# Performance work log

Measured on AMD Instinct MI355X. Metric: run time of the kernel, lower is better.

The kernel has to match this reference:

```python
import jax, jax.numpy as jnp
import numpy as np

B, EIN, GIN, LAT, E = 32768, 128, 64, 16, 8
H1, H2, H3 = 512, 256, 128          # CpExpertNet hidden_sizes
BB, GH = 128, 128                   # gate backbone_dim, gating_hidden_dim
EPS = 1e-5

def _ln(x, g, b):
    # LayerNorm over last dim (eps=1e-5, affine)
    mu = jnp.mean(x, axis=-1, keepdims=True)
    var = jnp.mean(jnp.square(x - mu), axis=-1, keepdims=True)
    return (x - mu) * jax.lax.rsqrt(var + EPS) * g + b

def setup_inputs() -> dict:
    key = jax.random.key(0)
    ks = iter(jax.random.split(key, 64))
    def p(shape, s=0.05):
        return jax.random.normal(next(ks), shape, jnp.float32) * s
    inp = dict(
        expert_features=jax.random.normal(next(ks), (B, EIN), jnp.float32),
        gate_features=jax.random.normal(next(ks), (B, GIN), jnp.float32),
        # stacked expert params (E parallel MLPs: in->512->256->128->1, LN after each hidden Linear)
        eW1=p((E, EIN, H1)), eb1=p((E, H1)), eg1=jnp.ones((E, H1), jnp.float32), ebt1=jnp.zeros((E, H1), jnp.float32),
        eW2=p((E, H1, H2)), eb2=p((E, H2)), eg2=jnp.ones((E, H2), jnp.float32), ebt2=jnp.zeros((E, H2), jnp.float32),
        eW3=p((E, H2, H3)), eb3=p((E, H3)), eg3=jnp.ones((E, H3), jnp.float32), ebt3=jnp.zeros((E, H3), jnp.float32),
        eW4=p((E, H3, 1)), eb4=p((E, 1)),
        # gate backbone: Linear(GIN,BB)+LN+SiLU, Linear(BB,BB)+LN+SiLU
        bW1=p((GIN, BB)), bb1=p((BB,)), bg1=jnp.ones((BB,), jnp.float32), bbt1=jnp.zeros((BB,), jnp.float32),
        bW2=p((BB, BB)), bb2=p((BB,)), bg2=jnp.ones((BB,), jnp.float32), bbt2=jnp.zeros((BB,), jnp.float32),
        # encoder: Linear(BB,BB//2)+SiLU, Linear(BB//2,LAT)
        encW1=p((BB, BB // 2)), encb1=p((BB // 2,)), encW2=p((BB // 2, LAT)), encb2=p((LAT,)),
        # gating: Linear(BB+LAT,GH)+LN+SiLU+(Dropout eval), Linear(GH,GH//2)+SiLU, Linear(GH//2,E)
        gW1=p((BB + LAT, GH)), gb1=p((GH,)), gg1=jnp.ones((GH,), jnp.float32), gbt1=jnp.zeros((GH,), jnp.float32),
        gW2=p((GH, GH // 2)), gb2=p((GH // 2,)),
        gW3=p((GH // 2, E)), gb3=p((E,)),
    )
    return inp

def reference(expert_features, gate_features,
              eW1, eb1, eg1, ebt1, eW2, eb2, eg2, ebt2, eW3, eb3, eg3, ebt3, eW4, eb4,
              bW1, bb1, bg1, bbt1, bW2, bb2, bg2, bbt2,
              encW1, encb1, encW2, encb2,
              gW1, gb1, gg1, gbt1, gW2, gb2, gW3, gb3):
    silu = jax.nn.silu
    # --- LatentGateNet ---
    h = silu(_ln(gate_features @ bW1 + bb1, bg1, bbt1))
    h = silu(_ln(h @ bW2 + bb2, bg2, bbt2))            # [B, BB]
    z = silu(h @ encW1 + encb1) @ encW2 + encb2        # [B, LAT]
    g = silu(_ln(jnp.concatenate([h, z], axis=1) @ gW1 + gb1, gg1, gbt1))
    g = silu(g @ gW2 + gb2)
    logits = g @ gW3 + gb3                             # [B, E]
    gates = jax.nn.softmax(logits, axis=1)
    # --- experts, batched over E via einsum (dropout is identity in eval) ---
    x = silu(_ln(jnp.einsum('bi,eih->beh', expert_features, eW1) + eb1, eg1, ebt1))  # [B,E,512]
    x = silu(_ln(jnp.einsum('beh,ehk->bek', x, eW2) + eb2, eg2, ebt2))               # [B,E,256]
    x = silu(_ln(jnp.einsum('bek,ekm->bem', x, eW3) + eb3, eg3, ebt3))               # [B,E,128]
    out = jnp.einsum('bem,emo->beo', x, eW4) + eb4                                   # [B,E,1]
    stacked = jnp.transpose(out, (0, 2, 1))                                          # [B,1,E]
    mixed = jnp.sum(stacked * gates[:, None, :], axis=2)                             # [B,1]
    return (mixed, z, logits, gates)
```

## Files before the change

kernel.cpp:

```cpp
#include <hip/hip_runtime.h>
#include <hip/hip_bf16.h>


typedef __attribute__((ext_vector_type(8))) short bf16x8;
typedef __attribute__((ext_vector_type(4))) short bf16x4;
typedef __attribute__((ext_vector_type(4))) float f32x4;

#define DEV static __device__ __forceinline__

DEV float b2f(unsigned short u){ union { unsigned int i; float f; } x; x.i = ((unsigned int)u) << 16; return x.f; }
DEV unsigned short f2b(float f){
  union { float f; unsigned int i; } x; x.f = f;
  return (unsigned short)((x.i + 0x7fffu + ((x.i >> 16) & 1u)) >> 16);
}
DEV unsigned int pk2(float a, float b){
  __hip_bfloat162 h = __float22bfloat162_rn(make_float2(a, b));
  union { __hip_bfloat162 h; unsigned int u; } u; u.h = h; return u.u;
}
DEV float silu_f(float v){ return v / (1.0f + __expf(-v)); }


__global__ __launch_bounds__(256) void pack_x_kernel(const float* __restrict__ X, unsigned short* __restrict__ Xp){
  int t = blockIdx.x * 256 + threadIdx.x;
  int l = t & 63, kb = (t >> 6) & 3, mtg = t >> 8;
  int row = mtg * 16 + (l & 15);
  int k0  = kb * 32 + (l >> 4) * 8;
  const float* src = X + (size_t)row * 128 + k0;
  bf16x8 o;
  #pragma unroll
  for (int j = 0; j < 8; j++) o[j] = (short)f2b(src[j]);
  *(bf16x8*)(Xp + (size_t)t * 8) = o;
}

__global__ __launch_bounds__(256) void pack_w_kernel(const float* __restrict__ eW1, const float* __restrict__ eW2,
                                                     const float* __restrict__ eW3, const float* __restrict__ eW4,
                                                     unsigned short* __restrict__ W1p, unsigned short* __restrict__ W2p,
                                                     unsigned short* __restrict__ W3p, float* __restrict__ w4p){
  int b = blockIdx.x;
  if (b < 256){
    int t = b * 256 + threadIdx.x;
    int l = t & 63, kb = (t >> 6) & 3, ntg = (t >> 8) & 31, e = t >> 13;
    int q = l >> 4, c0 = l & 15, n = ntg * 16 + c0;
    bf16x8 o;
    #pragma unroll
    for (int j = 0; j < 8; j++){ int k = kb*32 + q*8 + j; o[j] = (short)f2b(eW1[((size_t)e*128 + k)*512 + n]); }
    *(bf16x8*)(W1p + (size_t)t * 8) = o;
  } else if (b < 768){
    int t = (b - 256) * 256 + threadIdx.x;
    int l = t & 63, kb = (t >> 6) & 15, ntg = (t >> 10) & 15, e = t >> 14;
    int q = l >> 4, c0 = l & 15, n = ntg * 16 + c0;
    bf16x8 o;
    #pragma unroll
    for (int j = 0; j < 8; j++){
      int kp = kb*32 + q*8 + j;
      int c = (kp >> 7) * 128 + (kp & 7) * 16 + ((kp >> 3) & 15);
      o[j] = (short)f2b(eW2[((size_t)e*512 + c)*256 + n]);
    }
    *(bf16x8*)(W2p + (size_t)t * 8) = o;
  } else if (b < 896){
    int t = (b - 768) * 256 + threadIdx.x;
    int l = t & 63, kb = (t >> 6) & 7, ntg = (t >> 9) & 7, e = t >> 12;
    int q = l >> 4, c0 = l & 15, n = ntg * 16 + c0;
    bf16x8 o;
    #pragma unroll
    for (int j = 0; j < 8; j++){
      int kp = kb*32 + q*8 + j;
      int c = (kp >> 6) * 64 + (kp & 3) * 16 + ((kp >> 2) & 15);
      o[j] = (short)f2b(eW3[((size_t)e*256 + c)*128 + n]);
    }
    *(bf16x8*)(W3p + (size_t)t * 8) = o;
  } else {
    int t = (b - 896) * 256 + threadIdx.x;
    if (t < 1024){
      int e = t >> 7, kp = t & 127;
      int c = (kp >> 5) * 32 + (kp & 1) * 16 + ((kp >> 1) & 15);
      w4p[t] = eW4[e * 128 + c];
    }
  }
}

#define MFMA_BF16 __builtin_amdgcn_mfma_f32_16x16x32_bf16

__global__ __launch_bounds__(256, 4)
void expert_kernel(const unsigned short* __restrict__ Xp,
                   const unsigned short* __restrict__ W1p,
                   const unsigned short* __restrict__ W2p,
                   const unsigned short* __restrict__ W3p,
                   const float* __restrict__ w4p,
                   const float* __restrict__ eb1, const float* __restrict__ eg1, const float* __restrict__ ebt1,
                   const float* __restrict__ eb2, const float* __restrict__ eg2, const float* __restrict__ ebt2,
                   const float* __restrict__ eb3, const float* __restrict__ eg3, const float* __restrict__ ebt3,
                   const float* __restrict__ eb4, float* __restrict__ eo)
{
  const int e = blockIdx.y, bt = blockIdx.x;
  const int tid = threadIdx.x;
  const int w = tid >> 6, l = tid & 63;
  const int q = l >> 4, c0 = l & 15;

  __shared__ __align__(16) unsigned short h1[32 * 520];
  __shared__ float redS[32 * 4];
  __shared__ float redQ[32 * 4];
  __shared__ float muS[32];
  __shared__ float rsS[32];
  unsigned short* h2 = h1;
  unsigned short* h3 = h1 + 32 * 264;

  {
    float bv[8], gv[8], tv[8];
    #pragma unroll
    for (int nt = 0; nt < 8; nt++){
      int col = w*128 + nt*16 + c0;
      bv[nt] = eb1[e*512 + col]; gv[nt] = eg1[e*512 + col]; tv[nt] = ebt1[e*512 + col];
    }
    f32x4 acc[2][8];
    #pragma unroll
    for (int m = 0; m < 2; m++)
      #pragma unroll
      for (int nt = 0; nt < 8; nt++) acc[m][nt] = (f32x4){bv[nt],bv[nt],bv[nt],bv[nt]};
    #pragma unroll
    for (int kb = 0; kb < 4; kb++){
      bf16x8 a0 = *(const bf16x8*)(Xp + ((size_t)((bt*2 + 0)*4 + kb)*64 + l)*8);
      bf16x8 a1 = *(const bf16x8*)(Xp + ((size_t)((bt*2 + 1)*4 + kb)*64 + l)*8);
      #pragma unroll
      for (int nt = 0; nt < 8; nt++){
        int ntg = w*8 + nt;
        bf16x8 b = *(const bf16x8*)(W1p + ((size_t)((e*32 + ntg)*4 + kb)*64 + l)*8);
        acc[0][nt] = MFMA_BF16(a0, b, acc[0][nt], 0, 0, 0);
        acc[1][nt] = MFMA_BF16(a1, b, acc[1][nt], 0, 0, 0);
      }
    }
    float s[2][4] = {}, sq[2][4] = {};
    #pragma unroll
    for (int nt = 0; nt < 8; nt++)
      #pragma unroll
      for (int m = 0; m < 2; m++)
        #pragma unroll
        for (int r = 0; r < 4; r++){
          float v = acc[m][nt][r];
          s[m][r] += v; sq[m][r] += v*v;
        }
    #pragma unroll
    for (int m = 0; m < 2; m++)
      #pragma unroll
      for (int r = 0; r < 4; r++){
        float a = s[m][r], b = sq[m][r];
        #pragma unroll
        for (int off = 1; off < 16; off <<= 1){ a += __shfl_xor(a, off, 64); b += __shfl_xor(b, off, 64); }
        if (c0 == 0){ int row = m*16 + q*4 + r; redS[row*4 + w] = a; redQ[row*4 + w] = b; }
      }
    __syncthreads();
    if (tid < 32){
      float S = 0.f, Q = 0.f;
      #pragma unroll
      for (int i = 0; i < 4; i++){ S += redS[tid*4 + i]; Q += redQ[tid*4 + i]; }
      float mu = S * (1.0f/512.0f);
      float var = Q * (1.0f/512.0f) - mu*mu;
      muS[tid] = mu; rsS[tid] = rsqrtf(var + 1e-5f);
    }
    __syncthreads();
    #pragma unroll
    for (int m = 0; m < 2; m++)
      #pragma unroll
      for (int r = 0; r < 4; r++){
        int row = m*16 + q*4 + r;
        float mu = muS[row], rs = rsS[row];
        float v[8];
        #pragma unroll
        for (int nt = 0; nt < 8; nt++) v[nt] = silu_f((acc[m][nt][r] - mu) * rs * gv[nt] + tv[nt]);
        uint4 pk;
        pk.x = pk2(v[0], v[1]); pk.y = pk2(v[2], v[3]); pk.z = pk2(v[4], v[5]); pk.w = pk2(v[6], v[7]);
        *(uint4*)(h1 + row*520 + w*128 + c0*8) = pk;
      }
  }
  __syncthreads();

  {
    float bv[4], gv[4], tv[4];
    #pragma unroll
    for (int nt = 0; nt < 4; nt++){
      int col = w*64 + nt*16 + c0;
      bv[nt] = eb2[e*256 + col]; gv[nt] = eg2[e*256 + col]; tv[nt] = ebt2[e*256 + col];
    }
    f32x4 acc[2][4];
    #pragma unroll
    for (int m = 0; m < 2; m++)
      #pragma unroll
      for (int nt = 0; nt < 4; nt++) acc[m][nt] = (f32x4){bv[nt],bv[nt],bv[nt],bv[nt]};
    #pragma unroll 2
    for (int kb = 0; kb < 16; kb++){
      bf16x8 a0 = *(const bf16x8*)(h1 + (0  + c0)*520 + kb*32 + q*8);
      bf16x8 a1 = *(const bf16x8*)(h1 + (16 + c0)*520 + kb*32 + q*8);
      #pragma unroll
      for (int nt = 0; nt < 4; nt++){
        int ntg = w*4 + nt;
        bf16x8 b = *(const bf16x8*)(W2p + ((size_t)((e*16 + ntg)*16 + kb)*64 + l)*8);
        acc[0][nt] = MFMA_BF16(a0, b, acc[0][nt], 0, 0, 0);
        acc[1][nt] = MFMA_BF16(a1, b, acc[1][nt], 0, 0, 0);
      }
    }
    float s[2][4] = {}, sq[2][4] = {};
    #pragma unroll
    for (int nt = 0; nt < 4; nt++)
      #pragma unroll
      for (int m = 0; m < 2; m++)
        #pragma unroll
        for (int r = 0; r < 4; r++){
          float v = acc[m][nt][r];
          s[m][r] += v; sq[m][r] += v*v;
        }
    #pragma unroll
    for (int m = 0; m < 2; m++)
      #pragma unroll
      for (int r = 0; r < 4; r++){
        float a = s[m][r], b = sq[m][r];
        #pragma unroll
        for (int off = 1; off < 16; off <<= 1){ a += __shfl_xor(a, off, 64); b += __shfl_xor(b, off, 64); }
        if (c0 == 0){ int row = m*16 + q*4 + r; redS[row*4 + w] = a; redQ[row*4 + w] = b; }
      }
    __syncthreads();
    if (tid < 32){
      float S = 0.f, Q = 0.f;
      #pragma unroll
      for (int i = 0; i < 4; i++){ S += redS[tid*4 + i]; Q += redQ[tid*4 + i]; }
      float mu = S * (1.0f/256.0f);
      float var = Q * (1.0f/256.0f) - mu*mu;
      muS[tid] = mu; rsS[tid] = rsqrtf(var + 1e-5f);
    }
    __syncthreads();
    #pragma unroll
    for (int m = 0; m < 2; m++)
      #pragma unroll
      for (int r = 0; r < 4; r++){
        int row = m*16 + q*4 + r;
        float mu = muS[row], rs = rsS[row];
        float v[4];
        #pragma unroll
        for (int nt = 0; nt < 4; nt++) v[nt] = silu_f((acc[m][nt][r] - mu) * rs * gv[nt] + tv[nt]);
        uint2 pk; pk.x = pk2(v[0], v[1]); pk.y = pk2(v[2], v[3]);
        *(uint2*)(h2 + row*264 + w*64 + c0*4) = pk;
      }
  }
  __syncthreads();

  {
    float bv[2], gv[2], tv[2];
    #pragma unroll
    for (int nt = 0; nt < 2; nt++){
      int col = w*32 + nt*16 + c0;
      bv[nt] = eb3[e*128 + col]; gv[nt] = eg3[e*128 + col]; tv[nt] = ebt3[e*128 + col];
    }
    f32x4 acc[2][2];
    #pragma unroll
    for (int m = 0; m < 2; m++)
      #pragma unroll
      for (int nt = 0; nt < 2; nt++) acc[m][nt] = (f32x4){bv[nt],bv[nt],bv[nt],bv[nt]};
    #pragma unroll 2
    for (int kb = 0; kb < 8; kb++){
      bf16x8 a0 = *(const bf16x8*)(h2 + (0  + c0)*264 + kb*32 + q*8);
      bf16x8 a1 = *(const bf16x8*)(h2 + (16 + c0)*264 + kb*32 + q*8);
      #pragma unroll
      for (int nt = 0; nt < 2; nt++){
        int ntg = w*2 + nt;
        bf16x8 b = *(const bf16x8*)(W3p + ((size_t)((e*8 + ntg)*8 + kb)*64 + l)*8);
        acc[0][nt] = MFMA_BF16(a0, b, acc[0][nt], 0, 0, 0);
        acc[1][nt] = MFMA_BF16(a1, b, acc[1][nt], 0, 0, 0);
      }
    }
    float s[2][4] = {}, sq[2][4] = {};
    #pragma unroll
    for (int nt = 0; nt < 2; nt++)
      #pragma unroll
      for (int m = 0; m < 2; m++)
        #pragma unroll
        for (int r = 0; r < 4; r++){
          float v = acc[m][nt][r];
          s[m][r] += v; sq[m][r] += v*v;
        }
    #pragma unroll
    for (int m = 0; m < 2; m++)
      #pragma unroll
      for (int r = 0; r < 4; r++){
        float a = s[m][r], b = sq[m][r];
        #pragma unroll
        for (int off = 1; off < 16; off <<= 1){ a += __shfl_xor(a, off, 64); b += __shfl_xor(b, off, 64); }
        if (c0 == 0){ int row = m*16 + q*4 + r; redS[row*4 + w] = a; redQ[row*4 + w] = b; }
      }
    __syncthreads();
    if (tid < 32){
      float S = 0.f, Q = 0.f;
      #pragma unroll
      for (int i = 0; i < 4; i++){ S += redS[tid*4 + i]; Q += redQ[tid*4 + i]; }
      float mu = S * (1.0f/128.0f);
      float var = Q * (1.0f/128.0f) - mu*mu;
      muS[tid] = mu; rsS[tid] = rsqrtf(var + 1e-5f);
    }
    __syncthreads();
    #pragma unroll
    for (int m = 0; m < 2; m++)
      #pragma unroll
      for (int r = 0; r < 4; r++){
        int row = m*16 + q*4 + r;
        float mu = muS[row], rs = rsS[row];
        float v0 = silu_f((acc[m][0][r] - mu) * rs * gv[0] + tv[0]);
        float v1 = silu_f((acc[m][1][r] - mu) * rs * gv[1] + tv[1]);
        *(unsigned int*)(h3 + row*136 + w*32 + c0*2) = pk2(v0, v1);
      }
  }
  __syncthreads();

  {
    int row = tid >> 3, sub = tid & 7;
    bf16x8 v0 = *(const bf16x8*)(h3 + row*136 + sub*16);
    bf16x8 v1 = *(const bf16x8*)(h3 + row*136 + sub*16 + 8);
    float a = 0.f;
    #pragma unroll
    for (int j = 0; j < 8; j++) a += b2f((unsigned short)v0[j]) * w4p[e*128 + sub*16 + j];
    #pragma unroll
    for (int j = 0; j < 8; j++) a += b2f((unsigned short)v1[j]) * w4p[e*128 + sub*16 + 8 + j];
    a += __shfl_xor(a, 1, 64); a += __shfl_xor(a, 2, 64); a += __shfl_xor(a, 4, 64);
    if (sub == 0) eo[(size_t)(bt*32 + row)*8 + e] = a + eb4[e];
  }
}

template<int K, int PIN, int POUT, bool LN>
DEV void glayer128(const float* __restrict__ xs, const float* __restrict__ W, const float* __restrict__ b,
                   const float* __restrict__ g, const float* __restrict__ btv, float* __restrict__ ys, int tid)
{
  const int cg = tid & 31, rg = tid >> 5;
  const int col0 = cg * 4, row0 = rg * 4;
  float4 bv = *(const float4*)(b + col0);
  float acc[4][4];
  #pragma unroll
  for (int r = 0; r < 4; r++){ acc[r][0] = bv.x; acc[r][1] = bv.y; acc[r][2] = bv.z; acc[r][3] = bv.w; }
  for (int k = 0; k < K; k += 4){
    float4 x0 = *(const float4*)(xs + (row0+0)*PIN + k);
    float4 x1 = *(const float4*)(xs + (row0+1)*PIN + k);
    float4 x2 = *(const float4*)(xs + (row0+2)*PIN + k);
    float4 x3 = *(const float4*)(xs + (row0+3)*PIN + k);
    float4 w0 = *(const float4*)(W + (size_t)(k+0)*128 + col0);
    float4 w1 = *(const float4*)(W + (size_t)(k+1)*128 + col0);
    float4 w2 = *(const float4*)(W + (size_t)(k+2)*128 + col0);
    float4 w3 = *(const float4*)(W + (size_t)(k+3)*128 + col0);
    const float xr[4][4] = {{x0.x,x0.y,x0.z,x0.w},{x1.x,x1.y,x1.z,x1.w},{x2.x,x2.y,x2.z,x2.w},{x3.x,x3.y,x3.z,x3.w}};
    const float wr[4][4] = {{w0.x,w0.y,w0.z,w0.w},{w1.x,w1.y,w1.z,w1.w},{w2.x,w2.y,w2.z,w2.w},{w3.x,w3.y,w3.z,w3.w}};
    #pragma unroll
    for (int kk = 0; kk < 4; kk++)
      #pragma unroll
      for (int r = 0; r < 4; r++)
        #pragma unroll
        for (int c = 0; c < 4; c++) acc[r][c] += xr[r][kk] * wr[kk][c];
  }
  float mu[4], rs[4];
  if (LN){
    #pragma unroll
    for (int r = 0; r < 4; r++){
      float s = acc[r][0] + acc[r][1] + acc[r][2] + acc[r][3];
      float qq = acc[r][0]*acc[r][0] + acc[r][1]*acc[r][1] + acc[r][2]*acc[r][2] + acc[r][3]*acc[r][3];
      #pragma unroll
      for (int off = 1; off < 32; off <<= 1){ s += __shfl_xor(s, off, 64); qq += __shfl_xor(qq, off, 64); }
      float m = s * (1.0f/128.0f);
      mu[r] = m; rs[r] = rsqrtf(qq * (1.0f/128.0f) - m*m + 1e-5f);
    }
    float4 gv = *(const float4*)(g + col0);
    float4 tv = *(const float4*)(btv + col0);
    const float gr[4] = {gv.x, gv.y, gv.z, gv.w};
    const float tr[4] = {tv.x, tv.y, tv.z, tv.w};
    #pragma unroll
    for (int r = 0; r < 4; r++)
      #pragma unroll
      for (int c = 0; c < 4; c++) acc[r][c] = (acc[r][c] - mu[r]) * rs[r] * gr[c] + tr[c];
  }
  #pragma unroll
  for (int r = 0; r < 4; r++){
    float4 o;
    o.x = silu_f(acc[r][0]); o.y = silu_f(acc[r][1]); o.z = silu_f(acc[r][2]); o.w = silu_f(acc[r][3]);
    *(float4*)(ys + (row0+r)*POUT + col0) = o;
  }
}

template<int K, int PIN, int POUT>
DEV void glayer64(const float* __restrict__ xs, const float* __restrict__ W, const float* __restrict__ b,
                  float* __restrict__ ys, int tid)
{
  const int cg = tid & 15, rg = tid >> 4;
  const int col0 = cg * 4, row0 = rg * 2;
  float4 bv = *(const float4*)(b + col0);
  float acc[2][4];
  #pragma unroll
  for (int r = 0; r < 2; r++){ acc[r][0] = bv.x; acc[r][1] = bv.y; acc[r][2] = bv.z; acc[r][3] = bv.w; }
  for (int k = 0; k < K; k += 4){
    float4 x0 = *(const float4*)(xs + (row0+0)*PIN + k);
    float4 x1 = *(const float4*)(xs + (row0+1)*PIN + k);
    float4 w0 = *(const float4*)(W + (size_t)(k+0)*64 + col0);
    float4 w1 = *(const float4*)(W + (size_t)(k+1)*64 + col0);
    float4 w2 = *(const float4*)(W + (size_t)(k+2)*64 + col0);
    float4 w3 = *(const float4*)(W + (size_t)(k+3)*64 + col0);
    const float xr[2][4] = {{x0.x,x0.y,x0.z,x0.w},{x1.x,x1.y,x1.z,x1.w}};
    const float wr[4][4] = {{w0.x,w0.y,w0.z,w0.w},{w1.x,w1.y,w1.z,w1.w},{w2.x,w2.y,w2.z,w2.w},{w3.x,w3.y,w3.z,w3.w}};
    #pragma unroll
    for (int kk = 0; kk < 4; kk++)
      #pragma unroll
      for (int r = 0; r < 2; r++)
        #pragma unroll
        for (int c = 0; c < 4; c++) acc[r][c] += xr[r][kk] * wr[kk][c];
  }
  #pragma unroll
  for (int r = 0; r < 2; r++){
    float4 o;
    o.x = silu_f(acc[r][0]); o.y = silu_f(acc[r][1]); o.z = silu_f(acc[r][2]); o.w = silu_f(acc[r][3]);
    *(float4*)(ys + (row0+r)*POUT + col0) = o;
  }
}

__global__ __launch_bounds__(256, 4)
void gate_fused(const float* __restrict__ gf,
                const float* __restrict__ bW1, const float* __restrict__ bb1, const float* __restrict__ bg1, const float* __restrict__ bbt1,
                const float* __restrict__ bW2, const float* __restrict__ bb2, const float* __restrict__ bg2, const float* __restrict__ bbt2,
                const float* __restrict__ encW1, const float* __restrict__ encb1, const float* __restrict__ encW2, const float* __restrict__ encb2,
                const float* __restrict__ gW1, const float* __restrict__ gb1, const float* __restrict__ gg1v, const float* __restrict__ gbt1,
                const float* __restrict__ gW2, const float* __restrict__ gb2, const float* __restrict__ gW3, const float* __restrict__ gb3,
                float* __restrict__ out_z, float* __restrict__ out_logits, float* __restrict__ out_gates)
{
  const int tid = threadIdx.x;
  const int row0 = blockIdx.x * 32;
  __shared__ __align__(16) float xa[32 * 148];
  __shared__ __align__(16) float xb[32 * 132];

  for (int idx = tid; idx < 32*64; idx += 256){
    int r = idx >> 6, k = idx & 63;
    xa[r*148 + k] = gf[(size_t)(row0 + r)*64 + k];
  }
  __syncthreads();
  glayer128<64, 148, 132, true>(xa, bW1, bb1, bg1, bbt1, xb, tid);
  __syncthreads();
  glayer128<128, 132, 148, true>(xb, bW2, bb2, bg2, bbt2, xa, tid);
  __syncthreads();
  glayer64<128, 148, 132>(xa, encW1, encb1, xb, tid);
  __syncthreads();
  {
    int col = tid & 15, rr = tid >> 4;
    float a0 = encb2[col], a1 = a0;
    for (int k = 0; k < 64; k++){
      float wv = encW2[k*16 + col];
      a0 += xb[(rr*2+0)*132 + k] * wv;
      a1 += xb[(rr*2+1)*132 + k] * wv;
    }
    out_z[(size_t)(row0 + rr*2+0)*16 + col] = a0;
    out_z[(size_t)(row0 + rr*2+1)*16 + col] = a1;
    xa[(rr*2+0)*148 + 128 + col] = a0;
    xa[(rr*2+1)*148 + 128 + col] = a1;
  }
  __syncthreads();
  glayer128<144, 148, 132, true>(xa, gW1, gb1, gg1v, gbt1, xb, tid);
  __syncthreads();
  glayer64<128, 132, 148>(xb, gW2, gb2, xa, tid);
  __syncthreads();
  {
    int col = tid & 7, rr = tid >> 3;
    float a = gb3[col];
    for (int k = 0; k < 64; k++) a += xa[rr*148 + k] * gW3[k*8 + col];
    out_logits[(size_t)(row0 + rr)*8 + col] = a;
    float m = a;
    m = fmaxf(m, __shfl_xor(m, 1, 64));
    m = fmaxf(m, __shfl_xor(m, 2, 64));
    m = fmaxf(m, __shfl_xor(m, 4, 64));
    float ex = __expf(a - m);
    float s = ex;
    s += __shfl_xor(s, 1, 64); s += __shfl_xor(s, 2, 64); s += __shfl_xor(s, 4, 64);
    out_gates[(size_t)(row0 + rr)*8 + col] = ex / s;
  }
}

__global__ __launch_bounds__(256) void mix_kernel(const float* __restrict__ eo, const float* __restrict__ gates,
                                                  float* __restrict__ mixed){
  int t = blockIdx.x * 256 + threadIdx.x;
  if (t < 32768){
    const float4* a = (const float4*)(eo + (size_t)t*8);
    const float4* gg = (const float4*)(gates + (size_t)t*8);
    float4 a0 = a[0], a1 = a[1], g0 = gg[0], g1 = gg[1];
    mixed[t] = a0.x*g0.x + a0.y*g0.y + a0.z*g0.z + a0.w*g0.w
             + a1.x*g1.x + a1.y*g1.y + a1.z*g1.z + a1.w*g1.w;
  }
}

extern "C" void kernel_launch(void* const* d_in, const int* in_sizes, int n_in,
                              void* d_out, int out_size, void* d_ws, size_t ws_size,
                              hipStream_t stream)
{
  if (n_in < 36 || in_sizes[0] != 32768*128 || out_size < 1081344) return;

  const float* expert_features = (const float*)d_in[0];
  const float* gate_features   = (const float*)d_in[1];
  const float* eW1 = (const float*)d_in[2];
  const float* eb1 = (const float*)d_in[3];
  const float* eg1 = (const float*)d_in[4];
  const float* ebt1= (const float*)d_in[5];
  const float* eW2 = (const float*)d_in[6];
  const float* eb2 = (const float*)d_in[7];
  const float* eg2 = (const float*)d_in[8];
  const float* ebt2= (const float*)d_in[9];
  const float* eW3 = (const float*)d_in[10];
  const float* eb3 = (const float*)d_in[11];
  const float* eg3 = (const float*)d_in[12];
  const float* ebt3= (const float*)d_in[13];
  const float* eW4 = (const float*)d_in[14];
  const float* eb4 = (const float*)d_in[15];
  const float* bW1 = (const float*)d_in[16];
  const float* bb1 = (const float*)d_in[17];
  const float* bg1 = (const float*)d_in[18];
  const float* bbt1= (const float*)d_in[19];
  const float* bW2 = (const float*)d_in[20];
  const float* bb2 = (const float*)d_in[21];
  const float* bg2 = (const float*)d_in[22];
  const float* bbt2= (const float*)d_in[23];
  const float* encW1 = (const float*)d_in[24];
  const float* encb1 = (const float*)d_in[25];
  const float* encW2 = (const float*)d_in[26];
  const float* encb2 = (const float*)d_in[27];
  const float* gW1 = (const float*)d_in[28];
  const float* gb1 = (const float*)d_in[29];
  const float* gg1 = (const float*)d_in[30];
  const float* gbt1= (const float*)d_in[31];
  const float* gW2 = (const float*)d_in[32];
  const float* gb2 = (const float*)d_in[33];
  const float* gW3 = (const float*)d_in[34];
  const float* gb3 = (const float*)d_in[35];

  float* out        = (float*)d_out;
  float* out_mixed  = out;
  float* out_z      = out + 32768;
  float* out_logits = out + 557056;
  float* out_gates  = out + 819200;

  char* ws = (char*)d_ws;
  size_t off = 0;
  auto walloc = [&](size_t bytes) -> char* { char* p = ws + off; off += (bytes + 255) & ~(size_t)255; return p; };
  unsigned short* Xp  = (unsigned short*)walloc((size_t)4194304 * 2);
  unsigned short* W1p = (unsigned short*)walloc((size_t)524288  * 2);
  unsigned short* W2p = (unsigned short*)walloc((size_t)1048576 * 2);
  unsigned short* W3p = (unsigned short*)walloc((size_t)262144  * 2);
  float*          w4p = (float*)walloc((size_t)1024 * 4);
  float*          eo  = (float*)walloc((size_t)262144 * 4);
  if (off > ws_size) return;

  pack_x_kernel<<<2048, 256, 0, stream>>>(expert_features, Xp);
  pack_w_kernel<<< 900, 256, 0, stream>>>(eW1, eW2, eW3, eW4, W1p, W2p, W3p, w4p);

  gate_fused<<<1024, 256, 0, stream>>>(gate_features,
                                       bW1, bb1, bg1, bbt1, bW2, bb2, bg2, bbt2,
                                       encW1, encb1, encW2, encb2,
                                       gW1, gb1, gg1, gbt1, gW2, gb2, gW3, gb3,
                                       out_z, out_logits, out_gates);

  expert_kernel<<<dim3(1024, 8), 256, 0, stream>>>(Xp, W1p, W2p, W3p, w4p,
                                                   eb1, eg1, ebt1, eb2, eg2, ebt2, eb3, eg3, ebt3,
                                                   eb4, eo);

  mix_kernel<<<128, 256, 0, stream>>>(eo, out_gates, out_mixed);
}
```

Measured before the change: 473.6 us.

## Merge gate network and expert MLP into one launch with shared LDS

The gate network kernel and the expert MLP kernel become a single launch with a ninth grid row. Blocks in that row run the gate body, while the other rows run the expert layers, and both use one static shared-memory buffer. This removes one kernel launch and the serialization between the gate and expert kernels, so the gate work can fill idle CUs alongside expert blocks. SiLU also switches from a divide to a hardware reciprocal. The gate path now inherits the larger LDS footprint and the register pressure of the expert path, which may lower its occupancy.

```diff
diff --git a/kernel.cpp b/kernel.cpp
--- a/kernel.cpp
+++ b/kernel.cpp
@@ -3,7 +3,6 @@
 
 
 typedef __attribute__((ext_vector_type(8))) short bf16x8;
-typedef __attribute__((ext_vector_type(4))) short bf16x4;
 typedef __attribute__((ext_vector_type(4))) float f32x4;
 
 #define DEV static __device__ __forceinline__
@@ -17,7 +16,7 @@
   __hip_bfloat162 h = __float22bfloat162_rn(make_float2(a, b));
   union { __hip_bfloat162 h; unsigned int u; } u; u.h = h; return u.u;
 }
-DEV float silu_f(float v){ return v / (1.0f + __expf(-v)); }
+DEV float silu_f(float v){ return v * __builtin_amdgcn_rcpf(1.0f + __expf(-v)); }
 
 
 __global__ __launch_bounds__(256) void pack_x_kernel(const float* __restrict__ X, unsigned short* __restrict__ Xp){
@@ -76,249 +75,6 @@
       int c = (kp >> 5) * 32 + (kp & 1) * 16 + ((kp >> 1) & 15);
       w4p[t] = eW4[e * 128 + c];
     }
-  }
-}
-
-#define MFMA_BF16 __builtin_amdgcn_mfma_f32_16x16x32_bf16
-
-__global__ __launch_bounds__(256, 4)
-void expert_kernel(const unsigned short* __restrict__ Xp,
-                   const unsigned short* __restrict__ W1p,
-                   const unsigned short* __restrict__ W2p,
-                   const unsigned short* __restrict__ W3p,
-                   const float* __restrict__ w4p,
-                   const float* __restrict__ eb1, const float* __restrict__ eg1, const float* __restrict__ ebt1,
-                   const float* __restrict__ eb2, const float* __restrict__ eg2, const float* __restrict__ ebt2,
-                   const float* __restrict__ eb3, const float* __restrict__ eg3, const float* __restrict__ ebt3,
-                   const float* __restrict__ eb4, float* __restrict__ eo)
-{
-  const int e = blockIdx.y, bt = blockIdx.x;
-  const int tid = threadIdx.x;
-  const int w = tid >> 6, l = tid & 63;
-  const int q = l >> 4, c0 = l & 15;
-
-  __shared__ __align__(16) unsigned short h1[32 * 520];
-  __shared__ float redS[32 * 4];
-  __shared__ float redQ[32 * 4];
-  __shared__ float muS[32];
-  __shared__ float rsS[32];
-  unsigned short* h2 = h1;
-  unsigned short* h3 = h1 + 32 * 264;
-
-  {
-    float bv[8], gv[8], tv[8];
-    #pragma unroll
-    for (int nt = 0; nt < 8; nt++){
-      int col = w*128 + nt*16 + c0;
-      bv[nt] = eb1[e*512 + col]; gv[nt] = eg1[e*512 + col]; tv[nt] = ebt1[e*512 + col];
-    }
-    f32x4 acc[2][8];
-    #pragma unroll
-    for (int m = 0; m < 2; m++)
-      #pragma unroll
-      for (int nt = 0; nt < 8; nt++) acc[m][nt] = (f32x4){bv[nt],bv[nt],bv[nt],bv[nt]};
-    #pragma unroll
-    for (int kb = 0; kb < 4; kb++){
-      bf16x8 a0 = *(const bf16x8*)(Xp + ((size_t)((bt*2 + 0)*4 + kb)*64 + l)*8);
-      bf16x8 a1 = *(const bf16x8*)(Xp + ((size_t)((bt*2 + 1)*4 + kb)*64 + l)*8);
-      #pragma unroll
-      for (int nt = 0; nt < 8; nt++){
-        int ntg = w*8 + nt;
-        bf16x8 b = *(const bf16x8*)(W1p + ((size_t)((e*32 + ntg)*4 + kb)*64 + l)*8);
-        acc[0][nt] = MFMA_BF16(a0, b, acc[0][nt], 0, 0, 0);
-        acc[1][nt] = MFMA_BF16(a1, b, acc[1][nt], 0, 0, 0);
-      }
-    }
-    float s[2][4] = {}, sq[2][4] = {};
-    #pragma unroll
-    for (int nt = 0; nt < 8; nt++)
-      #pragma unroll
-      for (int m = 0; m < 2; m++)
-        #pragma unroll
-        for (int r = 0; r < 4; r++){
-          float v = acc[m][nt][r];
-          s[m][r] += v; sq[m][r] += v*v;
-        }
-    #pragma unroll
-    for (int m = 0; m < 2; m++)
-      #pragma unroll
-      for (int r = 0; r < 4; r++){
-        float a = s[m][r], b = sq[m][r];
-        #pragma unroll
-        for (int off = 1; off < 16; off <<= 1){ a += __shfl_xor(a, off, 64); b += __shfl_xor(b, off, 64); }
-        if (c0 == 0){ int row = m*16 + q*4 + r; redS[row*4 + w] = a; redQ[row*4 + w] = b; }
-      }
-    __syncthreads();
-    if (tid < 32){
-      float S = 0.f, Q = 0.f;
-      #pragma unroll
-      for (int i = 0; i < 4; i++){ S += redS[tid*4 + i]; Q += redQ[tid*4 + i]; }
-      float mu = S * (1.0f/512.0f);
-      float var = Q * (1.0f/512.0f) - mu*mu;
-      muS[tid] = mu; rsS[tid] = rsqrtf(var + 1e-5f);
-    }
-    __syncthreads();
-    #pragma unroll
-    for (int m = 0; m < 2; m++)
-      #pragma unroll
-      for (int r = 0; r < 4; r++){
-        int row = m*16 + q*4 + r;
-        float mu = muS[row], rs = rsS[row];
-        float v[8];
-        #pragma unroll
-        for (int nt = 0; nt < 8; nt++) v[nt] = silu_f((acc[m][nt][r] - mu) * rs * gv[nt] + tv[nt]);
-        uint4 pk;
-        pk.x = pk2(v[0], v[1]); pk.y = pk2(v[2], v[3]); pk.z = pk2(v[4], v[5]); pk.w = pk2(v[6], v[7]);
-        *(uint4*)(h1 + row*520 + w*128 + c0*8) = pk;
-      }
-  }
-  __syncthreads();
-
-  {
-    float bv[4], gv[4], tv[4];
-    #pragma unroll
-    for (int nt = 0; nt < 4; nt++){
-      int col = w*64 + nt*16 + c0;
-      bv[nt] = eb2[e*256 + col]; gv[nt] = eg2[e*256 + col]; tv[nt] = ebt2[e*256 + col];
-    }
-    f32x4 acc[2][4];
-    #pragma unroll
-    for (int m = 0; m < 2; m++)
-      #pragma unroll
-      for (int nt = 0; nt < 4; nt++) acc[m][nt] = (f32x4){bv[nt],bv[nt],bv[nt],bv[nt]};
-    #pragma unroll 2
-    for (int kb = 0; kb < 16; kb++){
-      bf16x8 a0 = *(const bf16x8*)(h1 + (0  + c0)*520 + kb*32 + q*8);
-      bf16x8 a1 = *(const bf16x8*)(h1 + (16 + c0)*520 + kb*32 + q*8);
-      #pragma unroll
-      for (int nt = 0; nt < 4; nt++){
-        int ntg = w*4 + nt;
-        bf16x8 b = *(const bf16x8*)(W2p + ((size_t)((e*16 + ntg)*16 + kb)*64 + l)*8);
-        acc[0][nt] = MFMA_BF16(a0, b, acc[0][nt], 0, 0, 0);
-        acc[1][nt] = MFMA_BF16(a1, b, acc[1][nt], 0, 0, 0);
-      }
-    }
-    float s[2][4] = {}, sq[2][4] = {};
-    #pragma unroll
-    for (int nt = 0; nt < 4; nt++)
-      #pragma unroll
-      for (int m = 0; m < 2; m++)
-        #pragma unroll
-        for (int r = 0; r < 4; r++){
-          float v = acc[m][nt][r];
-          s[m][r] += v; sq[m][r] += v*v;
-        }
-    #pragma unroll
-    for (int m = 0; m < 2; m++)
-      #pragma unroll
-      for (int r = 0; r < 4; r++){
-        float a = s[m][r], b = sq[m][r];
-        #pragma unroll
-        for (int off = 1; off < 16; off <<= 1){ a += __shfl_xor(a, off, 64); b += __shfl_xor(b, off, 64); }
-        if (c0 == 0){ int row = m*16 + q*4 + r; redS[row*4 + w] = a; redQ[row*4 + w] = b; }
-      }
-    __syncthreads();
-    if (tid < 32){
-      float S = 0.f, Q = 0.f;
-      #pragma unroll
-      for (int i = 0; i < 4; i++){ S += redS[tid*4 + i]; Q += redQ[tid*4 + i]; }
-      float mu = S * (1.0f/256.0f);
-      float var = Q * (1.0f/256.0f) - mu*mu;
-      muS[tid] = mu; rsS[tid] = rsqrtf(var + 1e-5f);
-    }
-    __syncthreads();
-    #pragma unroll
-    for (int m = 0; m < 2; m++)
-      #pragma unroll
-      for (int r = 0; r < 4; r++){
-        int row = m*16 + q*4 + r;
-        float mu = muS[row], rs = rsS[row];
-        float v[4];
-        #pragma unroll
-        for (int nt = 0; nt < 4; nt++) v[nt] = silu_f((acc[m][nt][r] - mu) * rs * gv[nt] + tv[nt]);
-        uint2 pk; pk.x = pk2(v[0], v[1]); pk.y = pk2(v[2], v[3]);
-        *(uint2*)(h2 + row*264 + w*64 + c0*4) = pk;
-      }
-  }
-  __syncthreads();
-
-  {
-    float bv[2], gv[2], tv[2];
-    #pragma unroll
-    for (int nt = 0; nt < 2; nt++){
-      int col = w*32 + nt*16 + c0;
-      bv[nt] = eb3[e*128 + col]; gv[nt] = eg3[e*128 + col]; tv[nt] = ebt3[e*128 + col];
-    }
-    f32x4 acc[2][2];
-    #pragma unroll
-    for (int m = 0; m < 2; m++)
-      #pragma unroll
-      for (int nt = 0; nt < 2; nt++) acc[m][nt] = (f32x4){bv[nt],bv[nt],bv[nt],bv[nt]};
-    #pragma unroll 2
-    for (int kb = 0; kb < 8; kb++){
-      bf16x8 a0 = *(const bf16x8*)(h2 + (0  + c0)*264 + kb*32 + q*8);
-      bf16x8 a1 = *(const bf16x8*)(h2 + (16 + c0)*264 + kb*32 + q*8);
-      #pragma unroll
-      for (int nt = 0; nt < 2; nt++){
-        int ntg = w*2 + nt;
-        bf16x8 b = *(const bf16x8*)(W3p + ((size_t)((e*8 + ntg)*8 + kb)*64 + l)*8);
-        acc[0][nt] = MFMA_BF16(a0, b, acc[0][nt], 0, 0, 0);
-        acc[1][nt] = MFMA_BF16(a1, b, acc[1][nt], 0, 0, 0);
-      }
-    }
-    float s[2][4] = {}, sq[2][4] = {};
-    #pragma unroll
-    for (int nt = 0; nt < 2; nt++)
-      #pragma unroll
-      for (int m = 0; m < 2; m++)
-        #pragma unroll
-        for (int r = 0; r < 4; r++){
-          float v = acc[m][nt][r];
-          s[m][r] += v; sq[m][r] += v*v;
-        }
-    #pragma unroll
-    for (int m = 0; m < 2; m++)
-      #pragma unroll
-      for (int r = 0; r < 4; r++){
-        float a = s[m][r], b = sq[m][r];
-        #pragma unroll
-        for (int off = 1; off < 16; off <<= 1){ a += __shfl_xor(a, off, 64); b += __shfl_xor(b, off, 64); }
-        if (c0 == 0){ int row = m*16 + q*4 + r; redS[row*4 + w] = a; redQ[row*4 + w] = b; }
-      }
-    __syncthreads();
-    if (tid < 32){
-      float S = 0.f, Q = 0.f;
-      #pragma unroll
-      for (int i = 0; i < 4; i++){ S += redS[tid*4 + i]; Q += redQ[tid*4 + i]; }
-      float mu = S * (1.0f/128.0f);
-      float var = Q * (1.0f/128.0f) - mu*mu;
-      muS[tid] = mu; rsS[tid] = rsqrtf(var + 1e-5f);
-    }
-    __syncthreads();
-    #pragma unroll
-    for (int m = 0; m < 2; m++)
-      #pragma unroll
-      for (int r = 0; r < 4; r++){
-        int row = m*16 + q*4 + r;
-        float mu = muS[row], rs = rsS[row];
-        float v0 = silu_f((acc[m][0][r] - mu) * rs * gv[0] + tv[0]);
-        float v1 = silu_f((acc[m][1][r] - mu) * rs * gv[1] + tv[1]);
-        *(unsigned int*)(h3 + row*136 + w*32 + c0*2) = pk2(v0, v1);
-      }
-  }
-  __syncthreads();
-
-  {
-    int row = tid >> 3, sub = tid & 7;
-    bf16x8 v0 = *(const bf16x8*)(h3 + row*136 + sub*16);
-    bf16x8 v1 = *(const bf16x8*)(h3 + row*136 + sub*16 + 8);
-    float a = 0.f;
-    #pragma unroll
-    for (int j = 0; j < 8; j++) a += b2f((unsigned short)v0[j]) * w4p[e*128 + sub*16 + j];
-    #pragma unroll
-    for (int j = 0; j < 8; j++) a += b2f((unsigned short)v1[j]) * w4p[e*128 + sub*16 + 8 + j];
-    a += __shfl_xor(a, 1, 64); a += __shfl_xor(a, 2, 64); a += __shfl_xor(a, 4, 64);
-    if (sub == 0) eo[(size_t)(bt*32 + row)*8 + e] = a + eb4[e];
   }
 }
 
@@ -412,19 +168,18 @@
   }
 }
 
-__global__ __launch_bounds__(256, 4)
-void gate_fused(const float* __restrict__ gf,
-                const float* __restrict__ bW1, const float* __restrict__ bb1, const float* __restrict__ bg1, const float* __restrict__ bbt1,
-                const float* __restrict__ bW2, const float* __restrict__ bb2, const float* __restrict__ bg2, const float* __restrict__ bbt2,
-                const float* __restrict__ encW1, const float* __restrict__ encb1, const float* __restrict__ encW2, const float* __restrict__ encb2,
-                const float* __restrict__ gW1, const float* __restrict__ gb1, const float* __restrict__ gg1v, const float* __restrict__ gbt1,
-                const float* __restrict__ gW2, const float* __restrict__ gb2, const float* __restrict__ gW3, const float* __restrict__ gb3,
-                float* __restrict__ out_z, float* __restrict__ out_logits, float* __restrict__ out_gates)
+DEV void gate_body(unsigned char* smem, int bx, int tid,
+                   const float* __restrict__ gf,
+                   const float* __restrict__ bW1, const float* __restrict__ bb1, const float* __restrict__ bg1, const float* __restrict__ bbt1,
+                   const float* __restrict__ bW2, const float* __restrict__ bb2, const float* __restrict__ bg2, const float* __restrict__ bbt2,
+                   const float* __restrict__ encW1, const float* __restrict__ encb1, const float* __restrict__ encW2, const float* __restrict__ encb2,
+                   const float* __restrict__ gW1, const float* __restrict__ gb1, const float* __restrict__ gg1v, const float* __restrict__ gbt1,
+                   const float* __restrict__ gW2, const float* __restrict__ gb2, const float* __restrict__ gW3, const float* __restrict__ gb3,
+                   float* __restrict__ out_z, float* __restrict__ out_logits, float* __restrict__ out_gates)
 {
-  const int tid = threadIdx.x;
-  const int row0 = blockIdx.x * 32;
-  __shared__ __align__(16) float xa[32 * 148];
-  __shared__ __align__(16) float xb[32 * 132];
+  const int row0 = bx * 32;
+  float* xa = (float*)smem;
+  float* xb = (float*)(smem + 18944);
 
   for (int idx = tid; idx < 32*64; idx += 256){
     int r = idx >> 6, k = idx & 63;
@@ -468,6 +223,267 @@
     float s = ex;
     s += __shfl_xor(s, 1, 64); s += __shfl_xor(s, 2, 64); s += __shfl_xor(s, 4, 64);
     out_gates[(size_t)(row0 + rr)*8 + col] = ex / s;
+  }
+}
+
+#define MFMA_BF16 __builtin_amdgcn_mfma_f32_16x16x32_bf16
+
+__global__ __launch_bounds__(256, 4)
+void fused_main(const unsigned short* __restrict__ Xp,
+                const unsigned short* __restrict__ W1p,
+                const unsigned short* __restrict__ W2p,
+                const unsigned short* __restrict__ W3p,
+                const float* __restrict__ w4p,
+                const float* __restrict__ eb1, const float* __restrict__ eg1, const float* __restrict__ ebt1,
+                const float* __restrict__ eb2, const float* __restrict__ eg2, const float* __restrict__ ebt2,
+                const float* __restrict__ eb3, const float* __restrict__ eg3, const float* __restrict__ ebt3,
+                const float* __restrict__ eb4, float* __restrict__ eo,
+                const float* __restrict__ gf,
+                const float* __restrict__ bW1, const float* __restrict__ bb1, const float* __restrict__ bg1, const float* __restrict__ bbt1,
+                const float* __restrict__ bW2, const float* __restrict__ bb2, const float* __restrict__ bg2, const float* __restrict__ bbt2,
+                const float* __restrict__ encW1, const float* __restrict__ encb1, const float* __restrict__ encW2, const float* __restrict__ encb2,
+                const float* __restrict__ gW1, const float* __restrict__ gb1, const float* __restrict__ gg1v, const float* __restrict__ gbt1,
+                const float* __restrict__ gW2, const float* __restrict__ gb2, const float* __restrict__ gW3, const float* __restrict__ gb3,
+                float* __restrict__ out_z, float* __restrict__ out_logits, float* __restrict__ out_gates)
+{
+  __shared__ __align__(16) unsigned char smem[35840];
+  const int tid = threadIdx.x;
+
+  if (blockIdx.y == 8){
+    gate_body(smem, blockIdx.x, tid, gf,
+              bW1, bb1, bg1, bbt1, bW2, bb2, bg2, bbt2,
+              encW1, encb1, encW2, encb2,
+              gW1, gb1, gg1v, gbt1, gW2, gb2, gW3, gb3,
+              out_z, out_logits, out_gates);
+    return;
+  }
+
+  const int e = blockIdx.y, bt = blockIdx.x;
+  const int w = tid >> 6, l = tid & 63;
+  const int q = l >> 4, c0 = l & 15;
+
+  unsigned short* h1 = (unsigned short*)smem;
+  float* redS = (float*)(smem + 33280);
+  float* redQ = (float*)(smem + 33792);
+  float* muS  = (float*)(smem + 34304);
+  float* rsS  = (float*)(smem + 34432);
+  unsigned short* h2 = h1;
+  unsigned short* h3 = h1 + 32 * 264;
+
+  {
+    float bv[8], gv[8], tv[8];
+    #pragma unroll
+    for (int nt = 0; nt < 8; nt++){
+      int col = w*128 + nt*16 + c0;
+      bv[nt] = eb1[e*512 + col]; gv[nt] = eg1[e*512 + col]; tv[nt] = ebt1[e*512 + col];
+    }
+    f32x4 acc[2][8];
+    #pragma unroll
+    for (int m = 0; m < 2; m++)
+      #pragma unroll
+      for (int nt = 0; nt < 8; nt++) acc[m][nt] = (f32x4){bv[nt],bv[nt],bv[nt],bv[nt]};
+    #pragma unroll
+    for (int kb = 0; kb < 4; kb++){
+      bf16x8 a0 = *(const bf16x8*)(Xp + ((size_t)((bt*2 + 0)*4 + kb)*64 + l)*8);
+      bf16x8 a1 = *(const bf16x8*)(Xp + ((size_t)((bt*2 + 1)*4 + kb)*64 + l)*8);
+      #pragma unroll
+      for (int nt = 0; nt < 8; nt++){
+        int ntg = w*8 + nt;
+        bf16x8 b = *(const bf16x8*)(W1p + ((size_t)((e*32 + ntg)*4 + kb)*64 + l)*8);
+        acc[0][nt] = MFMA_BF16(a0, b, acc[0][nt], 0, 0, 0);
+        acc[1][nt] = MFMA_BF16(a1, b, acc[1][nt], 0, 0, 0);
+      }
+    }
+    float s[2][4] = {}, sq[2][4] = {};
+    #pragma unroll
+    for (int nt = 0; nt < 8; nt++)
+      #pragma unroll
+      for (int m = 0; m < 2; m++)
+        #pragma unroll
+        for (int r = 0; r < 4; r++){
+          float v = acc[m][nt][r];
+          s[m][r] += v; sq[m][r] += v*v;
+        }
+    #pragma unroll
+    for (int m = 0; m < 2; m++)
+      #pragma unroll
+      for (int r = 0; r < 4; r++){
+        float a = s[m][r], b = sq[m][r];
+        #pragma unroll
+        for (int off = 1; off < 16; off <<= 1){ a += __shfl_xor(a, off, 64); b += __shfl_xor(b, off, 64); }
+        if (c0 == 0){ int row = m*16 + q*4 + r; redS[row*4 + w] = a; redQ[row*4 + w] = b; }
+      }
+    __syncthreads();
+    if (tid < 32){
+      float S = 0.f, Q = 0.f;
+      #pragma unroll
+      for (int i = 0; i < 4; i++){ S += redS[tid*4 + i]; Q += redQ[tid*4 + i]; }
+      float mu = S * (1.0f/512.0f);
+      float var = Q * (1.0f/512.0f) - mu*mu;
+      muS[tid] = mu; rsS[tid] = rsqrtf(var + 1e-5f);
+    }
+    __syncthreads();
+    #pragma unroll
+    for (int m = 0; m < 2; m++)
+      #pragma unroll
+      for (int r = 0; r < 4; r++){
+        int row = m*16 + q*4 + r;
+        float mu = muS[row], rs = rsS[row];
+        float v[8];
+        #pragma unroll
+        for (int nt = 0; nt < 8; nt++) v[nt] = silu_f((acc[m][nt][r] - mu) * rs * gv[nt] + tv[nt]);
+        uint4 pk;
+        pk.x = pk2(v[0], v[1]); pk.y = pk2(v[2], v[3]); pk.z = pk2(v[4], v[5]); pk.w = pk2(v[6], v[7]);
+        *(uint4*)(h1 + row*520 + w*128 + c0*8) = pk;
+      }
+  }
+  __syncthreads();
+
+  {
+    float bv[4], gv[4], tv[4];
+    #pragma unroll
+    for (int nt = 0; nt < 4; nt++){
+      int col = w*64 + nt*16 + c0;
+      bv[nt] = eb2[e*256 + col]; gv[nt] = eg2[e*256 + col]; tv[nt] = ebt2[e*256 + col];
+    }
+    f32x4 acc[2][4];
+    #pragma unroll
+    for (int m = 0; m < 2; m++)
+      #pragma unroll
+      for (int nt = 0; nt < 4; nt++) acc[m][nt] = (f32x4){bv[nt],bv[nt],bv[nt],bv[nt]};
+    #pragma unroll 2
+    for (int kb = 0; kb < 16; kb++){
+      bf16x8 a0 = *(const bf16x8*)(h1 + (0  + c0)*520 + kb*32 + q*8);
+      bf16x8 a1 = *(const bf16x8*)(h1 + (16 + c0)*520 + kb*32 + q*8);
+      #pragma unroll
+      for (int nt = 0; nt < 4; nt++){
+        int ntg = w*4 + nt;
+        bf16x8 b = *(const bf16x8*)(W2p + ((size_t)((e*16 + ntg)*16 + kb)*64 + l)*8);
+        acc[0][nt] = MFMA_BF16(a0, b, acc[0][nt], 0, 0, 0);
+        acc[1][nt] = MFMA_BF16(a1, b, acc[1][nt], 0, 0, 0);
+      }
+    }
+    float s[2][4] = {}, sq[2][4] = {};
+    #pragma unroll
+    for (int nt = 0; nt < 4; nt++)
+      #pragma unroll
+      for (int m = 0; m < 2; m++)
+        #pragma unroll
+        for (int r = 0; r < 4; r++){
+          float v = acc[m][nt][r];
+          s[m][r] += v; sq[m][r] += v*v;
+        }
+    #pragma unroll
+    for (int m = 0; m < 2; m++)
+      #pragma unroll
+      for (int r = 0; r < 4; r++){
+        float a = s[m][r], b = sq[m][r];
+        #pragma unroll
+        for (int off = 1; off < 16; off <<= 1){ a += __shfl_xor(a, off, 64); b += __shfl_xor(b, off, 64); }
+        if (c0 == 0){ int row = m*16 + q*4 + r; redS[row*4 + w] = a; redQ[row*4 + w] = b; }
+      }
+    __syncthreads();
+    if (tid < 32){
+      float S = 0.f, Q = 0.f;
+      #pragma unroll
+      for (int i = 0; i < 4; i++){ S += redS[tid*4 + i]; Q += redQ[tid*4 + i]; }
+      float mu = S * (1.0f/256.0f);
+      float var = Q * (1.0f/256.0f) - mu*mu;
+      muS[tid] = mu; rsS[tid] = rsqrtf(var + 1e-5f);
+    }
+    __syncthreads();
+    #pragma unroll
+    for (int m = 0; m < 2; m++)
+      #pragma unroll
+      for (int r = 0; r < 4; r++){
+        int row = m*16 + q*4 + r;
+        float mu = muS[row], rs = rsS[row];
+        float v[4];
+        #pragma unroll
+        for (int nt = 0; nt < 4; nt++) v[nt] = silu_f((acc[m][nt][r] - mu) * rs * gv[nt] + tv[nt]);
+        uint2 pk; pk.x = pk2(v[0], v[1]); pk.y = pk2(v[2], v[3]);
+        *(uint2*)(h2 + row*264 + w*64 + c0*4) = pk;
+      }
+  }
+  __syncthreads();
+
+  {
+    float bv[2], gv[2], tv[2];
+    #pragma unroll
+    for (int nt = 0; nt < 2; nt++){
+      int col = w*32 + nt*16 + c0;
+      bv[nt] = eb3[e*128 + col]; gv[nt] = eg3[e*128 + col]; tv[nt] = ebt3[e*128 + col];
+    }
+    f32x4 acc[2][2];
+    #pragma unroll
+    for (int m = 0; m < 2; m++)
+      #pragma unroll
+      for (int nt = 0; nt < 2; nt++) acc[m][nt] = (f32x4){bv[nt],bv[nt],bv[nt],bv[nt]};
+    #pragma unroll 2
+    for (int kb = 0; kb < 8; kb++){
+      bf16x8 a0 = *(const bf16x8*)(h2 + (0  + c0)*264 + kb*32 + q*8);
+      bf16x8 a1 = *(const bf16x8*)(h2 + (16 + c0)*264 + kb*32 + q*8);
+      #pragma unroll
+      for (int nt = 0; nt < 2; nt++){
+        int ntg = w*2 + nt;
+        bf16x8 b = *(const bf16x8*)(W3p + ((size_t)((e*8 + ntg)*8 + kb)*64 + l)*8);
+        acc[0][nt] = MFMA_BF16(a0, b, acc[0][nt], 0, 0, 0);
+        acc[1][nt] = MFMA_BF16(a1, b, acc[1][nt], 0, 0, 0);
+      }
+    }
+    float s[2][4] = {}, sq[2][4] = {};
+    #pragma unroll
+    for (int nt = 0; nt < 2; nt++)
+      #pragma unroll
+      for (int m = 0; m < 2; m++)
+        #pragma unroll
+        for (int r = 0; r < 4; r++){
+          float v = acc[m][nt][r];
+          s[m][r] += v; sq[m][r] += v*v;
+        }
+    #pragma unroll
+    for (int m = 0; m < 2; m++)
+      #pragma unroll
+      for (int r = 0; r < 4; r++){
+        float a = s[m][r], b = sq[m][r];
+        #pragma unroll
+        for (int off = 1; off < 16; off <<= 1){ a += __shfl_xor(a, off, 64); b += __shfl_xor(b, off, 64); }
+        if (c0 == 0){ int row = m*16 + q*4 + r; redS[row*4 + w] = a; redQ[row*4 + w] = b; }
+      }
+    __syncthreads();
+    if (tid < 32){
+      float S = 0.f, Q = 0.f;
+      #pragma unroll
+      for (int i = 0; i < 4; i++){ S += redS[tid*4 + i]; Q += redQ[tid*4 + i]; }
+      float mu = S * (1.0f/128.0f);
+      float var = Q * (1.0f/128.0f) - mu*mu;
+      muS[tid] = mu; rsS[tid] = rsqrtf(var + 1e-5f);
+    }
+    __syncthreads();
+    #pragma unroll
+    for (int m = 0; m < 2; m++)
+      #pragma unroll
+      for (int r = 0; r < 4; r++){
+        int row = m*16 + q*4 + r;
+        float mu = muS[row], rs = rsS[row];
+        float v0 = silu_f((acc[m][0][r] - mu) * rs * gv[0] + tv[0]);
+        float v1 = silu_f((acc[m][1][r] - mu) * rs * gv[1] + tv[1]);
+        *(unsigned int*)(h3 + row*136 + w*32 + c0*2) = pk2(v0, v1);
+      }
+  }
+  __syncthreads();
+
+  {
+    int row = tid >> 3, sub = tid & 7;
+    bf16x8 v0 = *(const bf16x8*)(h3 + row*136 + sub*16);
+    bf16x8 v1 = *(const bf16x8*)(h3 + row*136 + sub*16 + 8);
+    float a = 0.f;
+    #pragma unroll
+    for (int j = 0; j < 8; j++) a += b2f((unsigned short)v0[j]) * w4p[e*128 + sub*16 + j];
+    #pragma unroll
+    for (int j = 0; j < 8; j++) a += b2f((unsigned short)v1[j]) * w4p[e*128 + sub*16 + 8 + j];
+    a += __shfl_xor(a, 1, 64); a += __shfl_xor(a, 2, 64); a += __shfl_xor(a, 4, 64);
+    if (sub == 0) eo[(size_t)(bt*32 + row)*8 + e] = a + eb4[e];
   }
 }
 
@@ -546,15 +562,14 @@
   pack_x_kernel<<<2048, 256, 0, stream>>>(expert_features, Xp);
   pack_w_kernel<<< 900, 256, 0, stream>>>(eW1, eW2, eW3, eW4, W1p, W2p, W3p, w4p);
 
-  gate_fused<<<1024, 256, 0, stream>>>(gate_features,
-                                       bW1, bb1, bg1, bbt1, bW2, bb2, bg2, bbt2,
-                                       encW1, encb1, encW2, encb2,
-                                       gW1, gb1, gg1, gbt1, gW2, gb2, gW3, gb3,
-                                       out_z, out_logits, out_gates);
-
-  expert_kernel<<<dim3(1024, 8), 256, 0, stream>>>(Xp, W1p, W2p, W3p, w4p,
-                                                   eb1, eg1, ebt1, eb2, eg2, ebt2, eb3, eg3, ebt3,
-                                                   eb4, eo);
+  fused_main<<<dim3(1024, 9), 256, 0, stream>>>(Xp, W1p, W2p, W3p, w4p,
+                                                eb1, eg1, ebt1, eb2, eg2, ebt2, eb3, eg3, ebt3,
+                                                eb4, eo,
+                                                gate_features,
+                                                bW1, bb1, bg1, bbt1, bW2, bb2, bg2, bbt2,
+                                                encW1, encb1, encW2, encb2,
+                                                gW1, gb1, gg1, gbt1, gW2, gb2, gW3, gb3,
+                                                out_z, out_logits, out_gates);
 
   mix_kernel<<<128, 256, 0, stream>>>(eo, out_gates, out_mixed);
 }
```

Result: faster. 435.4 us (-8.1%).
